# Optimization experiments

Hardware: AMD Instinct MI355X
Metric: run time of the kernel (lower is better)

Reference implementation:

```python
import jax, jax.numpy as jnp
import numpy as np

EMB = 1024
HEADS = 16
HEADSIZE = EMB // HEADS


def _layernorm(x, gamma, beta, eps=1e-5):
    # LayerNorm over the last dim (headsize), affine.
    mu = jnp.mean(x, axis=-1, keepdims=True)
    var = jnp.var(x, axis=-1, keepdims=True)
    return (x - mu) * jax.lax.rsqrt(var + eps) * gamma + beta


def setup_inputs() -> dict:
    key = jax.random.key(0)
    ks = jax.random.split(key, 12)
    B, TI, TC = 4, 1024, 1024
    s = 1.0 / np.sqrt(EMB)
    inp = {
        "x": jax.random.normal(ks[0], (B, TI, EMB), dtype=jnp.float32),
        "context": jax.random.normal(ks[1], (B, TC, EMB), dtype=jnp.float32),
        # torch nn.Linear weights are (out, in); y = x @ W.T
        "Wq": jax.random.uniform(ks[2], (EMB, EMB), jnp.float32, -s, s),
        "Wk": jax.random.uniform(ks[3], (EMB, EMB), jnp.float32, -s, s),
        "Wv": jax.random.uniform(ks[4], (EMB, EMB), jnp.float32, -s, s),
        "Wu": jax.random.uniform(ks[5], (EMB, EMB), jnp.float32, -s, s),
        "bu": jax.random.uniform(ks[6], (EMB,), jnp.float32, -s, s),
        "q_gamma": jnp.ones((HEADSIZE,), jnp.float32),
        "q_beta": jnp.zeros((HEADSIZE,), jnp.float32),
        "k_gamma": jnp.ones((HEADSIZE,), jnp.float32),
        "k_beta": jnp.zeros((HEADSIZE,), jnp.float32),
    }
    return inp


def reference(x, context, Wq, Wk, Wv, Wu, bu, q_gamma, q_beta, k_gamma, k_beta):
    B, TI, E = x.shape
    TC = context.shape[1]
    T = TI + TC
    xc = jnp.concatenate([x, context], axis=1)  # [B, T, E]

    q = (x @ Wq.T).reshape(B, TI, HEADS, HEADSIZE)
    k = (xc @ Wk.T).reshape(B, T, HEADS, HEADSIZE)
    v = (xc @ Wv.T).reshape(B, T, HEADS, HEADSIZE)

    # optional QK-LayerNorm over headsize
    q = _layernorm(q, q_gamma, q_beta)
    k = _layernorm(k, k_gamma, k_beta)

    scale = E ** 0.25
    q = q / scale
    k = k / scale

    # scores: [B, H, TI, T]
    dot = jnp.einsum("bihd,bjhd->bhij", q, k)
    attn = jax.nn.softmax(dot, axis=-1)
    out = jnp.einsum("bhij,bjhd->bihd", attn, v).reshape(B, TI, E)
    return out @ Wu.T + bu
```

## Files before the change

kernel.cpp:

```cpp
#include <hip/hip_runtime.h>
#include <cstdint>


typedef unsigned short u16;
typedef __attribute__((ext_vector_type(8))) short bf16x8;
typedef __attribute__((ext_vector_type(4))) float f32x4;
typedef __attribute__((ext_vector_type(16))) float f32x16;
typedef __attribute__((ext_vector_type(4))) unsigned short u16x4;

#define GLDS(gsrc, ldst)                                                              \
  __builtin_amdgcn_global_load_lds(                                                   \
      (const __attribute__((address_space(1))) unsigned int*)(gsrc),                  \
      (__attribute__((address_space(3))) unsigned int*)(ldst), 16, 0, 0)

__device__ __forceinline__ u16 f2bf(float x) {
  unsigned int u = __float_as_uint(x);
  u += 0x7fffu + ((u >> 16) & 1u);
  return (u16)(u >> 16);
}

__device__ __forceinline__ f32x4 mfma16(bf16x8 a, bf16x8 b, f32x4 c) {
  return __builtin_amdgcn_mfma_f32_16x16x32_bf16(a, b, c, 0, 0, 0);
}
__device__ __forceinline__ f32x16 mfma32(bf16x8 a, bf16x8 b, f32x16 c) {
  return __builtin_amdgcn_mfma_f32_32x32x16_bf16(a, b, c, 0, 0, 0);
}


__global__ __launch_bounds__(256) void cast_concat(const float* __restrict__ x,
                                                   const float* __restrict__ c,
                                                   u16* __restrict__ o) {
  const int n4 = (8 << 20) / 4;
  for (int i = blockIdx.x * blockDim.x + threadIdx.x; i < n4; i += gridDim.x * blockDim.x) {
    int elem = i * 4;
    int b = elem >> 21;
    int rem = elem & ((1 << 21) - 1);
    int r = rem >> 10;
    int e = rem & 1023;
    const float* src = (r < 1024) ? (x + ((((size_t)(b << 10)) + r) << 10) + e)
                                  : (c + ((((size_t)(b << 10)) + (r - 1024)) << 10) + e);
    float4 v = *(const float4*)src;
    u16x4 ov;
    ov.x = f2bf(v.x); ov.y = f2bf(v.y); ov.z = f2bf(v.z); ov.w = f2bf(v.w);
    *(u16x4*)(o + elem) = ov;
  }
}

__global__ __launch_bounds__(256) void cast_w(const float* __restrict__ w0,
                                              const float* __restrict__ w1,
                                              const float* __restrict__ w2,
                                              const float* __restrict__ w3,
                                              u16* __restrict__ o) {
  const int n4 = (4 << 20) / 4;
  for (int i = blockIdx.x * blockDim.x + threadIdx.x; i < n4; i += gridDim.x * blockDim.x) {
    int elem = i * 4;
    int sel = elem >> 20;
    int loc = elem & ((1 << 20) - 1);
    const float* s = (sel == 0) ? w0 : (sel == 1) ? w1 : (sel == 2) ? w2 : w3;
    float4 v = *(const float4*)(s + loc);
    u16x4 ov;
    ov.x = f2bf(v.x); ov.y = f2bf(v.y); ov.z = f2bf(v.z); ov.w = f2bf(v.w);
    *(u16x4*)(o + elem) = ov;
  }
}


template <int EPI>
__global__ __launch_bounds__(256)
void gemm_bt(const u16* __restrict__ A, const u16* __restrict__ Bw,
             u16* __restrict__ Ob, float* __restrict__ Of,
             const float* __restrict__ P0, const float* __restrict__ P1,
             int M, int N, int K, int rpbo, int rpbi, float oscale) {
  __shared__ alignas(16) u16 lA[2][128 * 32];
  __shared__ alignas(16) u16 lB[2][128 * 32];
  const int tid = threadIdx.x;
  const int wv = tid >> 6, l = tid & 63, g = l >> 4, c16 = l & 15;
  const int wr = wv >> 1, wc = wv & 1;
  const int m0 = blockIdx.x * 128, n0 = blockIdx.y * 128;
  const int arow0 = (m0 / rpbo) * rpbi + (m0 % rpbo);

  f32x4 acc[4][4];
  const f32x4 z4 = {0.f, 0.f, 0.f, 0.f};
#pragma unroll
  for (int i = 0; i < 4; ++i)
#pragma unroll
    for (int j = 0; j < 4; ++j) acc[i][j] = z4;

  const int srow = tid >> 2;
  const int scA = (tid & 3) ^ (srow & 3);
  const u16* aSrc = A + (size_t)(arow0 + srow) * K + scA * 8;
  const u16* bSrc = Bw + (size_t)(n0 + srow) * K + scA * 8;
  char* ldA = (char*)lA;
  char* ldB = (char*)lB;
  const int lof = wv * 1024;

  const int ksteps = K >> 5;
#define STAGE_G(bi, kof)                                   \
  {                                                        \
    char* dA = ldA + (bi)*8192 + lof;                      \
    char* dB = ldB + (bi)*8192 + lof;                      \
    GLDS(aSrc + (kof), dA);                                \
    GLDS(aSrc + (size_t)64 * K + (kof), dA + 4096);        \
    GLDS(bSrc + (kof), dB);                                \
    GLDS(bSrc + (size_t)64 * K + (kof), dB + 4096);        \
  }

  STAGE_G(0, 0);
  __syncthreads();
  int buf = 0;
  for (int kt = 0; kt < ksteps; ++kt) {
    if (kt + 1 < ksteps) STAGE_G(buf ^ 1, (kt + 1) << 5);
    const char* bA = ldA + buf * 8192;
    const char* bB = ldB + buf * 8192;
    bf16x8 af[4], bfr[4];
#pragma unroll
    for (int mi = 0; mi < 4; ++mi) {
      int row = wr * 64 + mi * 16 + c16;
      af[mi] = *(const bf16x8*)(bA + row * 64 + ((g * 16) ^ ((row & 3) << 4)));
    }
#pragma unroll
    for (int ni = 0; ni < 4; ++ni) {
      int row = wc * 64 + ni * 16 + c16;
      bfr[ni] = *(const bf16x8*)(bB + row * 64 + ((g * 16) ^ ((row & 3) << 4)));
    }
#pragma unroll
    for (int mi = 0; mi < 4; ++mi)
#pragma unroll
      for (int ni = 0; ni < 4; ++ni)
        acc[mi][ni] = mfma16(af[mi], bfr[ni], acc[mi][ni]);
    __syncthreads();
    buf ^= 1;
  }
#undef STAGE_G

  if constexpr (EPI == 2) {
#pragma unroll
    for (int ni = 0; ni < 4; ++ni) {
      int col = n0 + wc * 64 + ni * 16 + c16;
      float bv = P0[col];
#pragma unroll
      for (int mi = 0; mi < 4; ++mi) {
        int row = m0 + wr * 64 + mi * 16 + g * 4;
        float* dst = Of + (size_t)row * N + col;
#pragma unroll
        for (int r = 0; r < 4; ++r) dst[(size_t)r * N] = acc[mi][ni][r] + bv;
      }
    }
  } else if constexpr (EPI == 1) {
#pragma unroll
    for (int ni = 0; ni < 4; ++ni) {
      int col = n0 + wc * 64 + ni * 16 + c16;
      int hh = col >> 6, dd = col & 63;
#pragma unroll
      for (int mi = 0; mi < 4; ++mi) {
        int m = m0 + wr * 64 + mi * 16 + g * 4;
        int bb = m >> 11, tt = m & 2047;
        u16x4 o;
#pragma unroll
        for (int r = 0; r < 4; ++r) o[r] = f2bf(acc[mi][ni][r]);
        *(u16x4*)(Ob + ((size_t)((bb * 16 + hh) * 64 + dd)) * 2048 + tt) = o;
      }
    }
  } else {
#pragma unroll
    for (int mi = 0; mi < 4; ++mi) {
      float sum[4], sq[4];
#pragma unroll
      for (int r = 0; r < 4; ++r) {
        float s = 0.f, q = 0.f;
#pragma unroll
        for (int ni = 0; ni < 4; ++ni) {
          float v = acc[mi][ni][r];
          s += v;
          q += v * v;
        }
#pragma unroll
        for (int msk = 1; msk < 16; msk <<= 1) {
          s += __shfl_xor(s, msk);
          q += __shfl_xor(q, msk);
        }
        sum[r] = s;
        sq[r] = q;
      }
#pragma unroll
      for (int ni = 0; ni < 4; ++ni) {
        int dloc = ni * 16 + c16;
        int colg = n0 + wc * 64 + ni * 16 + c16;
        float gv = P0[dloc], bv = P1[dloc];
#pragma unroll
        for (int r = 0; r < 4; ++r) {
          float mean = sum[r] * (1.f / 64.f);
          float var = sq[r] * (1.f / 64.f) - mean * mean;
          float y = (acc[mi][ni][r] - mean) * rsqrtf(var + 1e-5f) * gv + bv;
          int row = m0 + wr * 64 + mi * 16 + g * 4 + r;
          Ob[(size_t)row * N + colg] = f2bf(y * oscale);
        }
      }
    }
  }
}


__global__ __launch_bounds__(256)
void attn_kernel(const u16* __restrict__ Q, const u16* __restrict__ Kb,
                 const u16* __restrict__ Vt, u16* __restrict__ AO) {
  __shared__ alignas(16) u16 lK[2][4096];
  __shared__ alignas(16) u16 lV[2][4096];
  const int tid = threadIdx.x;
  const int wv = tid >> 6, l = tid & 63;
  const int lq = l & 31, hi = l >> 5;
  const int b = blockIdx.z, h = blockIdx.y, qt = blockIdx.x;
  const int qrow = (b << 10) + (qt << 7) + (wv << 5) + lq;

  const u16* qp = Q + (size_t)qrow * 1024 + h * 64 + hi * 8;
  bf16x8 qf[4];
#pragma unroll
  for (int kk = 0; kk < 4; ++kk) qf[kk] = *(const bf16x8*)(qp + 16 * kk);

  f32x16 acc[2];
#pragma unroll
  for (int d0 = 0; d0 < 2; ++d0)
#pragma unroll
    for (int i = 0; i < 16; ++i) acc[d0][i] = 0.f;
  float m_run = -1e30f, l_run = 0.f;

  const u16* Ksrc = Kb + ((size_t)(b * 2048) + l) * 1024 + h * 64 + wv * 8;
  const u16* Vsrc = Vt + ((size_t)((b * 16 + h) * 64) + l) * 2048 + wv * 8;
  char* ldK = (char*)lK;
  char* ldV = (char*)lV;

#define STAGE_KV(bi, kv0)                                  \
  {                                                        \
    char* dK = ldK + (bi)*8192 + wv * 1024;                \
    char* dV = ldV + (bi)*8192 + wv * 1024;                \
    const u16* ks = Ksrc + (size_t)(kv0) * 1024;           \
    const u16* vs = Vsrc + (kv0);                          \
    GLDS(ks, dK);                                          \
    GLDS(ks + 32, dK + 4096);                              \
    GLDS(vs, dV);                                          \
    GLDS(vs + 32, dV + 4096);                              \
  }

  STAGE_KV(0, 0);
  __syncthreads();
  int buf = 0;

  for (int t = 0; t < 32; ++t) {
    if (t + 1 < 32) STAGE_KV(buf ^ 1, (t + 1) << 6);
    const char* bK = ldK + buf * 8192;
    const char* bV = ldV + buf * 8192;

    f32x16 s[2];
#pragma unroll
    for (int kvh = 0; kvh < 2; ++kvh)
#pragma unroll
      for (int i = 0; i < 16; ++i) s[kvh][i] = 0.f;
    __builtin_amdgcn_s_setprio(1);
#pragma unroll
    for (int kk = 0; kk < 4; ++kk) {
      const char* kbase = bK + (2 * kk + hi) * 1024;
      bf16x8 kf0 = *(const bf16x8*)(kbase + lq * 16);
      bf16x8 kf1 = *(const bf16x8*)(kbase + (32 + lq) * 16);
      s[0] = mfma32(kf0, qf[kk], s[0]);
      s[1] = mfma32(kf1, qf[kk], s[1]);
    }
    __builtin_amdgcn_s_setprio(0);

    float tm = s[0][0];
#pragma unroll
    for (int i = 1; i < 16; ++i) tm = fmaxf(tm, s[0][i]);
#pragma unroll
    for (int i = 0; i < 16; ++i) tm = fmaxf(tm, s[1][i]);
    tm = fmaxf(tm, __shfl_xor(tm, 32));
    if (!__all(tm <= m_run + 8.f)) {
      float mnew = fmaxf(m_run, tm);
      float corr = exp2f(m_run - mnew);
      l_run *= corr;
#pragma unroll
      for (int d0 = 0; d0 < 2; ++d0)
#pragma unroll
        for (int i = 0; i < 16; ++i) acc[d0][i] *= corr;
      m_run = mnew;
    }
    float ts = 0.f;
#pragma unroll
    for (int kvh = 0; kvh < 2; ++kvh)
#pragma unroll
      for (int i = 0; i < 16; ++i) {
        float p = exp2f(s[kvh][i] - m_run);
        s[kvh][i] = p;
        ts += p;
      }
    ts += __shfl_xor(ts, 32);
    l_run += ts;

    unsigned int pk[2][4][2];
#pragma unroll
    for (int kvh = 0; kvh < 2; ++kvh)
#pragma unroll
      for (int kp = 0; kp < 4; ++kp)
#pragma unroll
        for (int tt = 0; tt < 2; ++tt)
          pk[kvh][kp][tt] = (unsigned)f2bf(s[kvh][4 * kp + 2 * tt]) |
                            ((unsigned)f2bf(s[kvh][4 * kp + 2 * tt + 1]) << 16);

#pragma unroll
    for (int kk = 0; kk < 4; ++kk) {
      const int kvh = kk >> 1, kb = kk & 1;
      union { unsigned w[4]; bf16x8 v; } bw;
#pragma unroll
      for (int tt = 0; tt < 2; ++tt) {
        unsigned A0 = pk[kvh][2 * kb][tt];
        unsigned A1 = pk[kvh][2 * kb + 1][tt];
        unsigned S = (unsigned)__shfl_xor((int)(hi ? A0 : A1), 32);
        bw.w[tt] = hi ? S : A0;
        bw.w[2 + tt] = hi ? A1 : S;
      }
      const char* vbase = bV + (2 * kk + hi) * 1024;
      bf16x8 vf0 = *(const bf16x8*)(vbase + lq * 16);
      bf16x8 vf1 = *(const bf16x8*)(vbase + (32 + lq) * 16);
      __builtin_amdgcn_s_setprio(1);
      acc[0] = mfma32(vf0, bw.v, acc[0]);
      acc[1] = mfma32(vf1, bw.v, acc[1]);
      __builtin_amdgcn_s_setprio(0);
    }
    __syncthreads();
    buf ^= 1;
  }
#undef STAGE_KV

  float invl = 1.f / l_run;
#pragma unroll
  for (int d0 = 0; d0 < 2; ++d0)
#pragma unroll
    for (int rg = 0; rg < 4; ++rg) {
      u16x4 o;
#pragma unroll
      for (int rr = 0; rr < 4; ++rr) o[rr] = f2bf(acc[d0][4 * rg + rr] * invl);
      int d = 32 * d0 + 8 * rg + 4 * hi;
      *(u16x4*)(AO + (size_t)qrow * 1024 + h * 64 + d) = o;
    }
}


extern "C" void kernel_launch(void* const* d_in, const int* in_sizes, int n_in,
                              void* d_out, int out_size, void* d_ws, size_t ws_size,
                              hipStream_t stream) {
  const float* x = (const float*)d_in[0];
  const float* ctx = (const float*)d_in[1];
  const float* Wq = (const float*)d_in[2];
  const float* Wk = (const float*)d_in[3];
  const float* Wv = (const float*)d_in[4];
  const float* Wu = (const float*)d_in[5];
  const float* bu = (const float*)d_in[6];
  const float* qg = (const float*)d_in[7];
  const float* qb = (const float*)d_in[8];
  const float* kg = (const float*)d_in[9];
  const float* kb = (const float*)d_in[10];
  float* out = (float*)d_out;

  char* w = (char*)d_ws;
  u16* XCB = (u16*)(w);
  u16* WQB = (u16*)(w + ((size_t)16 << 20));
  u16* WKB = (u16*)(w + ((size_t)18 << 20));
  u16* WVB = (u16*)(w + ((size_t)20 << 20));
  u16* WUB = (u16*)(w + ((size_t)22 << 20));
  u16* QBB = (u16*)(w + ((size_t)24 << 20));
  u16* KBB = (u16*)(w + ((size_t)32 << 20));
  u16* VT = (u16*)(w + ((size_t)48 << 20));
  u16* AO = (u16*)(w + ((size_t)64 << 20));

  const float invs = 0.17677669529663687f;
  const float invs_l2e = invs * 1.44269504088896f;

  cast_concat<<<2048, 256, 0, stream>>>(x, ctx, XCB);
  cast_w<<<1024, 256, 0, stream>>>(Wq, Wk, Wv, Wu, WQB);

  gemm_bt<0><<<dim3(32, 8), 256, 0, stream>>>(XCB, WQB, QBB, nullptr, qg, qb,
                                              4096, 1024, 1024, 1024, 2048, invs_l2e);
  gemm_bt<0><<<dim3(64, 8), 256, 0, stream>>>(XCB, WKB, KBB, nullptr, kg, kb,
                                              8192, 1024, 1024, 2048, 2048, invs);
  gemm_bt<1><<<dim3(64, 8), 256, 0, stream>>>(XCB, WVB, VT, nullptr, nullptr, nullptr,
                                              8192, 1024, 1024, 2048, 2048, 1.f);

  attn_kernel<<<dim3(8, 16, 4), 256, 0, stream>>>(QBB, KBB, VT, AO);

  gemm_bt<2><<<dim3(32, 8), 256, 0, stream>>>(AO, WUB, nullptr, out, bu, nullptr,
                                              4096, 1024, 1024, 4096, 4096, 1.f);
}
```

Measured before the change: 302.6 us.

## Split attention KV range across two wave groups with LDS merge of partial softmax

The attention kernel grows to 512 threads. Two groups of four waves each process half of the KV sequence, interleaved in 64-row chunks, with separate double-buffered LDS. At the end the partial accumulators and running max/sum are combined through shared memory. This adds parallelism per query tile to hide latency and raise occupancy, since the grid is only 512 blocks. It also uses the hardware packed bf16 convert and native exp2, and splits the max/sum reductions into independent chains. The cost is more LDS use plus an extra sync and combine step.

New measurement: 297.1 us. No clear change (-1.8%).

```diff
diff --git a/kernel.cpp b/kernel.cpp
--- a/kernel.cpp
+++ b/kernel.cpp
@@ -7,6 +7,7 @@
 typedef __attribute__((ext_vector_type(4))) float f32x4;
 typedef __attribute__((ext_vector_type(16))) float f32x16;
 typedef __attribute__((ext_vector_type(4))) unsigned short u16x4;
+typedef __attribute__((ext_vector_type(2))) unsigned int u32x2;
 
 #define GLDS(gsrc, ldst)                                                              \
   __builtin_amdgcn_global_load_lds(                                                   \
@@ -17,6 +18,12 @@
   unsigned int u = __float_as_uint(x);
   u += 0x7fffu + ((u >> 16) & 1u);
   return (u16)(u >> 16);
+}
+
+__device__ __forceinline__ unsigned cvt_pk_bf16(float lo, float hi) {
+  unsigned r;
+  asm("v_cvt_pk_bf16_f32 %0, %1, %2" : "=v"(r) : "v"(lo), "v"(hi));
+  return r;
 }
 
 __device__ __forceinline__ f32x4 mfma16(bf16x8 a, bf16x8 b, f32x4 c) {
@@ -201,16 +208,18 @@
 }
 
 
-__global__ __launch_bounds__(256)
+__global__ __launch_bounds__(512, 4)
 void attn_kernel(const u16* __restrict__ Q, const u16* __restrict__ Kb,
                  const u16* __restrict__ Vt, u16* __restrict__ AO) {
-  __shared__ alignas(16) u16 lK[2][4096];
-  __shared__ alignas(16) u16 lV[2][4096];
+  __shared__ alignas(16) u16 lK[2][2][4096];
+  __shared__ alignas(16) u16 lV[2][2][4096];
+  __shared__ float cmb[4][64][34];
   const int tid = threadIdx.x;
   const int wv = tid >> 6, l = tid & 63;
+  const int w4 = wv & 3, kvh2 = wv >> 2;
   const int lq = l & 31, hi = l >> 5;
   const int b = blockIdx.z, h = blockIdx.y, qt = blockIdx.x;
-  const int qrow = (b << 10) + (qt << 7) + (wv << 5) + lq;
+  const int qrow = (b << 10) + (qt << 7) + (w4 << 5) + lq;
 
   const u16* qp = Q + (size_t)qrow * 1024 + h * 64 + hi * 8;
   bf16x8 qf[4];
@@ -224,31 +233,30 @@
     for (int i = 0; i < 16; ++i) acc[d0][i] = 0.f;
   float m_run = -1e30f, l_run = 0.f;
 
-  const u16* Ksrc = Kb + ((size_t)(b * 2048) + l) * 1024 + h * 64 + wv * 8;
-  const u16* Vsrc = Vt + ((size_t)((b * 16 + h) * 64) + l) * 2048 + wv * 8;
-  char* ldK = (char*)lK;
-  char* ldV = (char*)lV;
-
-#define STAGE_KV(bi, kv0)                                  \
-  {                                                        \
-    char* dK = ldK + (bi)*8192 + wv * 1024;                \
-    char* dV = ldV + (bi)*8192 + wv * 1024;                \
-    const u16* ks = Ksrc + (size_t)(kv0) * 1024;           \
-    const u16* vs = Vsrc + (kv0);                          \
-    GLDS(ks, dK);                                          \
-    GLDS(ks + 32, dK + 4096);                              \
-    GLDS(vs, dV);                                          \
-    GLDS(vs + 32, dV + 4096);                              \
+  const u16* Ksrc = Kb + ((size_t)(b * 2048) + l) * 1024 + h * 64 + w4 * 8;
+  const u16* Vsrc = Vt + ((size_t)((b * 16 + h) * 64) + l) * 2048 + w4 * 8;
+
+#define STAGE_KV(bi, it)                                    \
+  {                                                         \
+    const int kv0 = ((it) << 7) + (kvh2 << 6);              \
+    char* dK = (char*)lK[kvh2][bi] + w4 * 1024;             \
+    char* dV = (char*)lV[kvh2][bi] + w4 * 1024;             \
+    const u16* ks = Ksrc + (size_t)kv0 * 1024;              \
+    const u16* vs = Vsrc + kv0;                             \
+    GLDS(ks, dK);                                           \
+    GLDS(ks + 32, dK + 4096);                               \
+    GLDS(vs, dV);                                           \
+    GLDS(vs + 32, dV + 4096);                               \
   }
 
   STAGE_KV(0, 0);
   __syncthreads();
   int buf = 0;
 
-  for (int t = 0; t < 32; ++t) {
-    if (t + 1 < 32) STAGE_KV(buf ^ 1, (t + 1) << 6);
-    const char* bK = ldK + buf * 8192;
-    const char* bV = ldV + buf * 8192;
+  for (int it = 0; it < 16; ++it) {
+    if (it + 1 < 16) STAGE_KV(buf ^ 1, it + 1);
+    const char* bK = (const char*)lK[kvh2][buf];
+    const char* bV = (const char*)lV[kvh2][buf];
 
     f32x16 s[2];
 #pragma unroll
@@ -266,15 +274,20 @@
     }
     __builtin_amdgcn_s_setprio(0);
 
-    float tm = s[0][0];
-#pragma unroll
-    for (int i = 1; i < 16; ++i) tm = fmaxf(tm, s[0][i]);
-#pragma unroll
-    for (int i = 0; i < 16; ++i) tm = fmaxf(tm, s[1][i]);
+    float tm0 = fmaxf(s[0][0], s[1][0]), tm1 = fmaxf(s[0][1], s[1][1]);
+    float tm2 = fmaxf(s[0][2], s[1][2]), tm3 = fmaxf(s[0][3], s[1][3]);
+#pragma unroll
+    for (int i = 4; i < 16; i += 4) {
+      tm0 = fmaxf(tm0, fmaxf(s[0][i], s[1][i]));
+      tm1 = fmaxf(tm1, fmaxf(s[0][i + 1], s[1][i + 1]));
+      tm2 = fmaxf(tm2, fmaxf(s[0][i + 2], s[1][i + 2]));
+      tm3 = fmaxf(tm3, fmaxf(s[0][i + 3], s[1][i + 3]));
+    }
+    float tm = fmaxf(fmaxf(tm0, tm1), fmaxf(tm2, tm3));
     tm = fmaxf(tm, __shfl_xor(tm, 32));
     if (!__all(tm <= m_run + 8.f)) {
       float mnew = fmaxf(m_run, tm);
-      float corr = exp2f(m_run - mnew);
+      float corr = __builtin_amdgcn_exp2f(m_run - mnew);
       l_run *= corr;
 #pragma unroll
       for (int d0 = 0; d0 < 2; ++d0)
@@ -282,15 +295,19 @@
         for (int i = 0; i < 16; ++i) acc[d0][i] *= corr;
       m_run = mnew;
     }
-    float ts = 0.f;
+    float ts0 = 0.f, ts1 = 0.f, ts2 = 0.f, ts3 = 0.f;
 #pragma unroll
     for (int kvh = 0; kvh < 2; ++kvh)
 #pragma unroll
-      for (int i = 0; i < 16; ++i) {
-        float p = exp2f(s[kvh][i] - m_run);
-        s[kvh][i] = p;
-        ts += p;
-      }
+      for (int i = 0; i < 16; i += 4) {
+        float p0 = __builtin_amdgcn_exp2f(s[kvh][i] - m_run);
+        float p1 = __builtin_amdgcn_exp2f(s[kvh][i + 1] - m_run);
+        float p2 = __builtin_amdgcn_exp2f(s[kvh][i + 2] - m_run);
+        float p3 = __builtin_amdgcn_exp2f(s[kvh][i + 3] - m_run);
+        s[kvh][i] = p0; s[kvh][i + 1] = p1; s[kvh][i + 2] = p2; s[kvh][i + 3] = p3;
+        ts0 += p0; ts1 += p1; ts2 += p2; ts3 += p3;
+      }
+    float ts = (ts0 + ts1) + (ts2 + ts3);
     ts += __shfl_xor(ts, 32);
     l_run += ts;
 
@@ -301,8 +318,7 @@
       for (int kp = 0; kp < 4; ++kp)
 #pragma unroll
         for (int tt = 0; tt < 2; ++tt)
-          pk[kvh][kp][tt] = (unsigned)f2bf(s[kvh][4 * kp + 2 * tt]) |
-                            ((unsigned)f2bf(s[kvh][4 * kp + 2 * tt + 1]) << 16);
+          pk[kvh][kp][tt] = cvt_pk_bf16(s[kvh][4 * kp + 2 * tt], s[kvh][4 * kp + 2 * tt + 1]);
 
 #pragma unroll
     for (int kk = 0; kk < 4; ++kk) {
@@ -329,17 +345,39 @@
   }
 #undef STAGE_KV
 
-  float invl = 1.f / l_run;
-#pragma unroll
-  for (int d0 = 0; d0 < 2; ++d0)
-#pragma unroll
-    for (int rg = 0; rg < 4; ++rg) {
-      u16x4 o;
-#pragma unroll
-      for (int rr = 0; rr < 4; ++rr) o[rr] = f2bf(acc[d0][4 * rg + rr] * invl);
-      int d = 32 * d0 + 8 * rg + 4 * hi;
-      *(u16x4*)(AO + (size_t)qrow * 1024 + h * 64 + d) = o;
-    }
+  if (wv >= 4) {
+    float* cp = cmb[w4][l];
+#pragma unroll
+    for (int d0 = 0; d0 < 2; ++d0)
+#pragma unroll
+      for (int i = 0; i < 16; ++i) cp[d0 * 16 + i] = acc[d0][i];
+    cp[32] = m_run;
+    cp[33] = l_run;
+  }
+  __syncthreads();
+  if (wv < 4) {
+    const float* cp = cmb[w4][l];
+    float m1 = cp[32], l1 = cp[33];
+    float mm = fmaxf(m_run, m1);
+    float c0 = __builtin_amdgcn_exp2f(m_run - mm);
+    float c1 = __builtin_amdgcn_exp2f(m1 - mm);
+    float invl = 1.f / (l_run * c0 + l1 * c1);
+    float s0 = c0 * invl, s1 = c1 * invl;
+#pragma unroll
+    for (int d0 = 0; d0 < 2; ++d0)
+#pragma unroll
+      for (int rg = 0; rg < 4; ++rg) {
+        float v0 = acc[d0][4 * rg + 0] * s0 + cp[d0 * 16 + 4 * rg + 0] * s1;
+        float v1 = acc[d0][4 * rg + 1] * s0 + cp[d0 * 16 + 4 * rg + 1] * s1;
+        float v2 = acc[d0][4 * rg + 2] * s0 + cp[d0 * 16 + 4 * rg + 2] * s1;
+        float v3 = acc[d0][4 * rg + 3] * s0 + cp[d0 * 16 + 4 * rg + 3] * s1;
+        u32x2 o;
+        o.x = cvt_pk_bf16(v0, v1);
+        o.y = cvt_pk_bf16(v2, v3);
+        int d = 32 * d0 + 8 * rg + 4 * hi;
+        *(u32x2*)(AO + (size_t)qrow * 1024 + h * 64 + d) = o;
+      }
+  }
 }
 
 
@@ -383,7 +421,7 @@
   gemm_bt<1><<<dim3(64, 8), 256, 0, stream>>>(XCB, WVB, VT, nullptr, nullptr, nullptr,
                                               8192, 1024, 1024, 2048, 2048, 1.f);
 
-  attn_kernel<<<dim3(8, 16, 4), 256, 0, stream>>>(QBB, KBB, VT, AO);
+  attn_kernel<<<dim3(8, 16, 4), 512, 0, stream>>>(QBB, KBB, VT, AO);
 
   gemm_bt<2><<<dim3(32, 8), 256, 0, stream>>>(AO, WUB, nullptr, out, bu, nullptr,
                                               4096, 1024, 1024, 4096, 4096, 1.f);
```
